# Performance work log

Hardware: AMD Instinct MI355X
Metric: run time of the kernel (lower is better)

Reference implementation:

```python
import jax, jax.numpy as jnp
import numpy as np

NV, NF, DIM = 6144, 12288, 256


def _linear(x, W, b):
    # torch nn.Linear: x @ W.T + b, W has shape (out, in)
    return x @ W.T + b


def _agg(X, A, Wf, bf, Wg, bg):
    # AGG: out_fc = Linear(A @ X); out_gagg = Linear(A @ out_fc)  (eval mode: dropout is identity)
    out_fc = _linear(A @ X, Wf, bf)
    out_g = _linear(A @ out_fc, Wg, bg)
    return jax.nn.relu(out_fc + out_g)


def setup_inputs() -> dict:
    key = jax.random.key(0)
    ks = jax.random.split(key, 18)
    primal = jax.random.normal(ks[0], (NV, DIM), jnp.float32)
    # degree-normalized adjacency (docstring): scale uniform entries by 1/N for stable row sums
    A_primal = jax.random.uniform(ks[1], (NV, NV), jnp.float32) * (1.0 / NV)
    A_dual = jax.random.uniform(ks[2], (NF, NF), jnp.float32) * (1.0 / NF)
    A = jax.random.uniform(ks[3], (NV, NF), jnp.float32) * (1.0 / NF)
    faces = jax.random.randint(ks[4], (NF, 3), 0, NV)

    w = lambda k, shp: jax.random.normal(k, shp, jnp.float32) * 0.05
    return {
        "primal": primal, "A_primal": A_primal, "A_dual": A_dual, "A": A, "faces": faces,
        # 3 primal AGG layers (fc + gagg), stacked on leading axis
        "pW": w(ks[5], (3, DIM, DIM)), "pb": w(ks[6], (3, DIM)),
        "pgW": w(ks[7], (3, DIM, DIM)), "pgb": w(ks[8], (3, DIM)),
        # 3 dual AGG layers
        "dW": w(ks[9], (3, DIM, DIM)), "db": w(ks[10], (3, DIM)),
        "dgW": w(ks[11], (3, DIM, DIM)), "dgb": w(ks[12], (3, DIM)),
        # PDF linears: (dim, 2*dim)
        "Wp": w(ks[13], (DIM, 2 * DIM)), "bp": w(ks[14], (DIM,)),
        "Wd": w(ks[15], (DIM, 2 * DIM)), "bd": w(ks[16], (DIM,)),
    }


def reference(primal, A_primal, A_dual, A, faces, pW, pb, pgW, pgb, dW, db, dgW, dgb, Wp, bp, Wd, bd):
    x_p = primal
    x_d = (1.0 / 3.0) * (A.T @ primal)  # primal_dual
    primal_outs, dual_outs = [], []
    for i in range(3):
        primal_outs.append(x_p)
        x_p = _agg(x_p, A_primal, pW[i], pb[i], pgW[i], pgb[i]) + x_p
    for i in range(3):
        dual_outs.append(x_d)
        x_d = _agg(x_d, A_dual, dW[i], db[i], dgW[i], dgb[i]) + x_d
    # PDF: DAP gather-reduce  (N_f, 3, dim) -> (N_f, dim)
    f = jnp.mean(jnp.abs(x_p[faces] - x_d[:, None, :]), axis=1)
    out_dual = jax.nn.relu(_linear(jnp.concatenate([x_d, f], axis=1), Wd, bd))
    mapped = A @ f  # dual_primal
    out_primal = jax.nn.relu(_linear(jnp.concatenate([x_p, mapped], axis=1), Wp, bp))
    return (out_primal + x_p, out_dual + x_d, *primal_outs, *dual_outs)
```

## Files before the change

### kernel.cpp

```cpp
#include <hip/hip_runtime.h>


typedef short short8 __attribute__((ext_vector_type(8)));
typedef float floatx4 __attribute__((ext_vector_type(4)));
typedef unsigned short ushort4v __attribute__((ext_vector_type(4)));
typedef unsigned short u16;

#define DIMN 256
#define GBK 64

static const int kNV = 6144;
static const int kNF = 12288;
static const int SLAB = 768;

__device__ __forceinline__ float bf2f(u16 u) {
  union { unsigned int i; float f; } x; x.i = ((unsigned int)u) << 16; return x.f;
}
__device__ __forceinline__ u16 f2bf(float f) {
  union { float f; unsigned int i; } x; x.f = f;
  unsigned int r = x.i + 0x7fffu + ((x.i >> 16) & 1u);
  return (u16)(r >> 16);
}
__device__ __forceinline__ void gld_lds16(const void* g, void* l) {
  __builtin_amdgcn_global_load_lds((__attribute__((address_space(1))) void*)(g),
                                   (__attribute__((address_space(3))) void*)(l),
                                   16, 0, 0);
}

struct GJ {
  const void* A0; int A0mode; int lda0;
  const void* A1; int A1mode; int lda1; int K1;
  const void* Bt; int Btis32; int ldb;
  u16* P; int M; int nx; int kchunk;
  int fused;
  const float* bias; const u16* addmat; int do_relu;
  const float* resid; float* outf; u16* out16; u16* outT;
};
struct FJ {
  const u16* P; int S; int Mrows; float scale; float* out; u16* out16;
};

__device__ __forceinline__ void gemm_dev(const GJ& j, int bid)
{
  __shared__ __align__(16) u16 As[2][128 * GBK];
  __shared__ __align__(16) u16 Bs[2][128 * GBK];

  const int y = bid & 1;
  const int bx = (bid >> 1) % j.nx;
  const int bz = (bid >> 1) / j.nx;
  const int m0 = bx << 7;
  const int n0 = y << 7;
  const int kb = bz * j.kchunk;
  const int nkt = j.kchunk / GBK;

  const int tid = threadIdx.x;
  const int wid = tid >> 6;
  const int lane = tid & 63;
  const int wr = wid >> 1, wc = wid & 1;
  const int srow = lane >> 3;
  const int skk = (lane & 7) << 3;

  floatx4 acc[4][4];
  floatx4 zz = {0.f, 0.f, 0.f, 0.f};
#pragma unroll
  for (int i = 0; i < 4; ++i)
#pragma unroll
    for (int jj = 0; jj < 4; ++jj) acc[i][jj] = zz;

  auto stage = [&](int buf, int k0) {
    const void* base; int lda, mode, kl;
    if (k0 < j.K1) { base = j.A0; lda = j.lda0; mode = j.A0mode; kl = k0; }
    else           { base = j.A1; lda = j.lda1; mode = j.A1mode; kl = k0 - j.K1; }
    if (mode == 0) {
      const u16* U = (const u16*)base;
#pragma unroll
      for (int q = 0; q < 4; ++q) {
        int c = (wid << 2) + q;
        gld_lds16(U + (size_t)(m0 + (c << 3) + srow) * lda + kl + skk,
                  (void*)&As[buf][c << 9]);
      }
    } else {
      const float* F = (const float*)base;
#pragma unroll
      for (int q = 0; q < 4; ++q) {
        int c = (wid << 2) + q;
        const size_t gi = (size_t)(m0 + (c << 3) + srow) * lda + kl + skk;
        floatx4 f0 = *(const floatx4*)(F + gi);
        floatx4 f1 = *(const floatx4*)(F + gi + 4);
        short8 v;
#pragma unroll
        for (int e = 0; e < 4; ++e) { v[e] = (short)f2bf(f0[e]); v[4 + e] = (short)f2bf(f1[e]); }
        *(short8*)&As[buf][(c << 9) + (lane << 3)] = v;
      }
    }
    if (j.Btis32) {
      const float* F = (const float*)j.Bt;
#pragma unroll
      for (int q = 0; q < 4; ++q) {
        int c = (wid << 2) + q;
        const size_t gi = (size_t)(n0 + (c << 3) + srow) * j.ldb + k0 + skk;
        floatx4 f0 = *(const floatx4*)(F + gi);
        floatx4 f1 = *(const floatx4*)(F + gi + 4);
        short8 v;
#pragma unroll
        for (int e = 0; e < 4; ++e) { v[e] = (short)f2bf(f0[e]); v[4 + e] = (short)f2bf(f1[e]); }
        *(short8*)&Bs[buf][(c << 9) + (lane << 3)] = v;
      }
    } else {
      const u16* U = (const u16*)j.Bt;
#pragma unroll
      for (int q = 0; q < 4; ++q) {
        int c = (wid << 2) + q;
        gld_lds16(U + (size_t)(n0 + (c << 3) + srow) * j.ldb + k0 + skk,
                  (void*)&Bs[buf][c << 9]);
      }
    }
  };

  int cur = 0;
  stage(0, kb);
  for (int kt = 0; kt < nkt; ++kt) {
    __syncthreads();
    if (kt + 1 < nkt) stage(cur ^ 1, kb + (kt + 1) * GBK);
#pragma unroll
    for (int ks = 0; ks < 2; ++ks) {
      short8 a[4], b[4];
      const int ko = (ks << 5) + ((lane >> 4) << 3);
#pragma unroll
      for (int mi = 0; mi < 4; ++mi)
        a[mi] = *(const short8*)&As[cur][((wr << 6) + (mi << 4) + (lane & 15)) * GBK + ko];
#pragma unroll
      for (int ni = 0; ni < 4; ++ni)
        b[ni] = *(const short8*)&Bs[cur][((wc << 6) + (ni << 4) + (lane & 15)) * GBK + ko];
#pragma unroll
      for (int mi = 0; mi < 4; ++mi)
#pragma unroll
        for (int ni = 0; ni < 4; ++ni)
          acc[mi][ni] = __builtin_amdgcn_mfma_f32_16x16x32_bf16(a[mi], b[ni], acc[mi][ni], 0, 0, 0);
    }
    cur ^= 1;
  }

  if (j.fused) {
    u16* ts = (u16*)&As[0][0];
    if (j.outT) __syncthreads();
#pragma unroll
    for (int mi = 0; mi < 4; ++mi) {
#pragma unroll
      for (int ni = 0; ni < 4; ++ni) {
        const int ml0 = (wr << 6) + (mi << 4) + ((lane >> 4) << 2);
        const int nl = (wc << 6) + (ni << 4) + (lane & 15);
        const int n = n0 + nl;
        const float bv = j.bias ? j.bias[n] : 0.f;
#pragma unroll
        for (int r = 0; r < 4; ++r) {
          const int ml = ml0 + r;
          const size_t idx = (size_t)(m0 + ml) * DIMN + n;
          float t = acc[mi][ni][r] + bv;
          if (j.addmat) t += bf2f(j.addmat[idx]);
          if (j.do_relu) t = fmaxf(t, 0.f);
          if (j.resid) t += j.resid[idx];
          if (j.outf) j.outf[idx] = t;
          const u16 q = f2bf(t);
          if (j.out16) j.out16[idx] = q;
          if (j.outT) ts[ml * 128 + (nl ^ ((ml & 7) << 3))] = q;
        }
      }
    }
    if (j.outT) {
      __syncthreads();
      const int nl = tid >> 1;
      const int mh = (tid & 1) << 6;
#pragma unroll
      for (int c8 = 0; c8 < 8; ++c8) {
        const int mB = mh + (c8 << 3);
        short8 v;
#pragma unroll
        for (int e = 0; e < 8; ++e)
          v[e] = (short)ts[(mB + e) * 128 + (nl ^ (((mB + e) & 7) << 3))];
        *(short8*)&j.outT[(size_t)(n0 + nl) * j.M + (m0 + mB)] = v;
      }
    }
  } else {
    u16* Pz = j.P + (size_t)bz * (size_t)j.M * DIMN;
#pragma unroll
    for (int mi = 0; mi < 4; ++mi) {
#pragma unroll
      for (int ni = 0; ni < 4; ++ni) {
        const int mb = m0 + (wr << 6) + (mi << 4) + ((lane >> 4) << 2);
        const int n = n0 + (wc << 6) + (ni << 4) + (lane & 15);
#pragma unroll
        for (int r = 0; r < 4; ++r)
          Pz[(size_t)(mb + r) * DIMN + n] = f2bf(acc[mi][ni][r]);
      }
    }
  }
}

__global__ __launch_bounds__(256, 2) void gemm1_k(GJ j0) { gemm_dev(j0, blockIdx.x); }
__global__ __launch_bounds__(256, 2) void gemm2_k(GJ j0, GJ j1, int nb0) {
  if ((int)blockIdx.x < nb0) gemm_dev(j0, blockIdx.x);
  else                       gemm_dev(j1, blockIdx.x - nb0);
}

__device__ __forceinline__ void fin_dev(const FJ& f, int bid)
{
  const size_t MN = (size_t)f.Mrows * DIMN;
  const size_t i4 = (((size_t)bid << 8) + threadIdx.x) * 4;
  if (i4 >= MN) return;
  floatx4 v = {0.f, 0.f, 0.f, 0.f};
  for (int s = 0; s < f.S; ++s) {
    ushort4v p4 = *(const ushort4v*)(f.P + (size_t)s * MN + i4);
#pragma unroll
    for (int q = 0; q < 4; ++q) v[q] += bf2f(p4[q]);
  }
  floatx4 o;
#pragma unroll
  for (int q = 0; q < 4; ++q) o[q] = v[q] * f.scale;
  if (f.out) *(floatx4*)(f.out + i4) = o;
  if (f.out16) {
    unsigned long long qq = 0;
#pragma unroll
    for (int q = 0; q < 4; ++q) qq |= ((unsigned long long)f2bf(o[q])) << (16 * q);
    *(unsigned long long*)(f.out16 + i4) = qq;
  }
}
__global__ __launch_bounds__(256) void fin1_k(FJ f0) { fin_dev(f0, blockIdx.x); }
__global__ __launch_bounds__(256) void fin2_k(FJ f0, FJ f1, int nb0) {
  if ((int)blockIdx.x < nb0) fin_dev(f0, blockIdx.x);
  else                       fin_dev(f1, blockIdx.x - nb0);
}

__global__ __launch_bounds__(256)
void finalize_tr_k(const u16* __restrict__ P, int S, int Mrows, float scale,
                   float* __restrict__ outf, u16* __restrict__ outT, int ldT)
{
  __shared__ __align__(16) u16 t[64][64];
  const size_t MN = (size_t)Mrows * DIMN;
  const int r0 = blockIdx.x << 6;
  const int c0 = blockIdx.y << 6;
  const int tid = threadIdx.x;
  const int lr = tid >> 3;
  const int lc = (tid & 7) << 3;
#pragma unroll
  for (int h = 0; h < 2; ++h) {
    const int r = lr + (h << 5);
    const size_t gi = (size_t)(r0 + r) * DIMN + (c0 + lc);
    float a[8];
#pragma unroll
    for (int e = 0; e < 8; ++e) a[e] = 0.f;
    for (int s = 0; s < S; ++s) {
      short8 p = *(const short8*)(P + (size_t)s * MN + gi);
#pragma unroll
      for (int e = 0; e < 8; ++e) a[e] += bf2f((u16)p[e]);
    }
    short8 v;
    floatx4 o0, o1;
#pragma unroll
    for (int e = 0; e < 4; ++e) {
      o0[e] = a[e] * scale; o1[e] = a[4 + e] * scale;
      v[e] = (short)f2bf(o0[e]); v[4 + e] = (short)f2bf(o1[e]);
    }
    *(floatx4*)(outf + gi) = o0;
    *(floatx4*)(outf + gi + 4) = o1;
    *(short8*)&t[r][lc ^ ((r >> 3) << 3)] = v;
  }
  __syncthreads();
#pragma unroll
  for (int h = 0; h < 2; ++h) {
    const int oc = lr + (h << 5);
    short8 v;
#pragma unroll
    for (int e = 0; e < 8; ++e)
      v[e] = (short)t[lc + e][oc ^ ((lc >> 3) << 3)];
    *(short8*)&outT[(size_t)(c0 + oc) * ldT + (r0 + lc)] = v;
  }
}

__device__ __forceinline__ void transpose_dev(const void* in, int is32, int ldin,
                                              u16* out, int ldout, u16* copy16,
                                              int bx, int by)
{
  __shared__ __align__(16) u16 t[64][64];
  const int c0 = bx << 6;
  const int r0 = by << 6;
  const int tid = threadIdx.x;
  const int lr = tid >> 3;
  const int lc = (tid & 7) << 3;
#pragma unroll
  for (int h = 0; h < 2; ++h) {
    const int r = lr + (h << 5);
    short8 v;
    if (is32) {
      const float* F = (const float*)in;
      const size_t gi = (size_t)(r0 + r) * ldin + (c0 + lc);
      floatx4 f0 = *(const floatx4*)(F + gi);
      floatx4 f1 = *(const floatx4*)(F + gi + 4);
#pragma unroll
      for (int e = 0; e < 4; ++e) { v[e] = (short)f2bf(f0[e]); v[4 + e] = (short)f2bf(f1[e]); }
      if (copy16) *(short8*)(copy16 + gi) = v;
    } else {
      v = *(const short8*)((const u16*)in + (size_t)(r0 + r) * ldin + (c0 + lc));
    }
    *(short8*)&t[r][lc ^ ((r >> 3) << 3)] = v;
  }
  __syncthreads();
#pragma unroll
  for (int h = 0; h < 2; ++h) {
    const int oc = lr + (h << 5);
    short8 v;
#pragma unroll
    for (int e = 0; e < 8; ++e)
      v[e] = (short)t[lc + e][oc ^ ((lc >> 3) << 3)];
    *(short8*)&out[(size_t)(c0 + oc) * ldout + (r0 + lc)] = v;
  }
}

__global__ __launch_bounds__(256)
void transpose_k(const void* __restrict__ in, int is32, int ldin,
                 u16* __restrict__ out, int ldout, u16* __restrict__ copy16)
{
  transpose_dev(in, is32, ldin, out, ldout, copy16, blockIdx.x, blockIdx.y);
}

__device__ __forceinline__ void cvt_dev(const float* in, u16* out, size_t n,
                                        int bid, int nb)
{
  const size_t stride = (size_t)nb * 2048;
  for (size_t i = (((size_t)bid << 8) + threadIdx.x) << 3; i < n; i += stride) {
    floatx4 f0 = *(const floatx4*)(in + i);
    floatx4 f1 = *(const floatx4*)(in + i + 4);
    short8 v;
#pragma unroll
    for (int e = 0; e < 4; ++e) { v[e] = (short)f2bf(f0[e]); v[4 + e] = (short)f2bf(f1[e]); }
    *(short8*)(out + i) = v;
  }
}
__global__ __launch_bounds__(256)
void prep_k(const float* __restrict__ Ad, u16* __restrict__ Ad16,
            const float* __restrict__ Ap, u16* __restrict__ Ap16,
            const float* __restrict__ A, u16* __restrict__ At16, u16* __restrict__ A16,
            const float* __restrict__ primal, u16* __restrict__ XTp,
            float* __restrict__ pouts)
{
  const int bid = blockIdx.x;
  if (bid < 2048) {
    cvt_dev(Ad, Ad16, (size_t)kNF * kNF, bid, 2048);
  } else if (bid < 3072) {
    cvt_dev(Ap, Ap16, (size_t)kNV * kNV, bid - 2048, 1024);
  } else if (bid < 21504) {
    const int t = bid - 3072;
    transpose_dev(A, 1, kNF, At16, kNV, A16, t % 192, t / 192);
  } else if (bid < 21888) {
    const int t = bid - 21504;
    transpose_dev(primal, 1, DIMN, XTp, kNV, nullptr, t % 4, t / 4);
  } else {
    const int t = bid - 21888;
    const size_t i = (((size_t)t << 8) + threadIdx.x) << 3;
    *(floatx4*)(pouts + i) = *(const floatx4*)(primal + i);
    *(floatx4*)(pouts + i + 4) = *(const floatx4*)(primal + i + 4);
  }
}

__global__ __launch_bounds__(256)
void face_gather_tr_k(const float* __restrict__ xp, const float* __restrict__ xd,
                      const int* __restrict__ faces, u16* __restrict__ f,
                      u16* __restrict__ fT)
{
  __shared__ u16 tile[64][DIMN + 8];
  const int fi0 = blockIdx.x << 6;
  const int jj = threadIdx.x;
  for (int k = 0; k < 64; ++k) {
    const int fi = fi0 + k;
    const int a = faces[fi * 3 + 0];
    const int b = faces[fi * 3 + 1];
    const int c = faces[fi * 3 + 2];
    const float xv = xd[(size_t)fi * DIMN + jj];
    const float s = fabsf(xp[(size_t)a * DIMN + jj] - xv)
                  + fabsf(xp[(size_t)b * DIMN + jj] - xv)
                  + fabsf(xp[(size_t)c * DIMN + jj] - xv);
    const u16 q = f2bf(s * (1.0f / 3.0f));
    f[(size_t)fi * DIMN + jj] = q;
    tile[k][jj] = q;
  }
  __syncthreads();
#pragma unroll
  for (int c8 = 0; c8 < 8; ++c8) {
    short8 v;
#pragma unroll
    for (int e = 0; e < 8; ++e) v[e] = (short)tile[(c8 << 3) + e][jj];
    *(short8*)&fT[(size_t)jj * kNF + fi0 + (c8 << 3)] = v;
  }
}

extern "C" void kernel_launch(void* const* d_in, const int* in_sizes, int n_in,
                              void* d_out, int out_size, void* d_ws, size_t ws_size,
                              hipStream_t stream)
{
  (void)in_sizes; (void)n_in; (void)out_size;
  const float* primal   = (const float*)d_in[0];
  const float* A_primal = (const float*)d_in[1];
  const float* A_dual   = (const float*)d_in[2];
  const float* A        = (const float*)d_in[3];
  const int* faces      = (const int*)d_in[4];
  const float* pW  = (const float*)d_in[5];
  const float* pb  = (const float*)d_in[6];
  const float* pgW = (const float*)d_in[7];
  const float* pgb = (const float*)d_in[8];
  const float* dW  = (const float*)d_in[9];
  const float* db  = (const float*)d_in[10];
  const float* dgW = (const float*)d_in[11];
  const float* dgb = (const float*)d_in[12];
  const float* Wp  = (const float*)d_in[13];
  const float* bp  = (const float*)d_in[14];
  const float* Wd  = (const float*)d_in[15];
  const float* bd  = (const float*)d_in[16];

  char* wsp = (char*)d_ws;
  auto alloc = [&](size_t bytes) -> void* {
    void* p = (void*)wsp;
    wsp += (bytes + 255) & ~(size_t)255;
    return p;
  };
  const size_t NVD = (size_t)kNV * DIMN, NFD = (size_t)kNF * DIMN;
  u16* XTp   = (u16*)alloc(NVD * 2);
  u16* XTd   = (u16*)alloc(NFD * 2);
  u16* TBd   = (u16*)alloc(NFD * 2);
  u16* TBp   = (u16*)alloc(NVD * 2);
  u16* t1d   = (u16*)alloc(NFD * 2);
  u16* t1p   = (u16*)alloc(NVD * 2);
  u16* fcd   = (u16*)alloc(NFD * 2);
  u16* fcp   = (u16*)alloc(NVD * 2);
  float* xp3 = (float*)alloc(NVD * 4);
  float* xd3 = (float*)alloc(NFD * 4);
  u16* P     = (u16*)alloc((size_t)8 * NFD * 2);
  u16* Pd    = P;
  u16* Pp    = P + 4 * NFD;
  const size_t bigElems = (size_t)kNF * kNF + 2 * (size_t)kNF * kNV + (size_t)kNV * kNV;
  const size_t need = (size_t)(wsp - (char*)d_ws) + bigElems * 2 + 4096;
  const bool big = ws_size >= need;
  u16 *Ad16 = nullptr, *At16 = nullptr, *A16 = nullptr, *Ap16 = nullptr;
  if (big) {
    Ad16 = (u16*)alloc((size_t)kNF * kNF * 2);
    At16 = (u16*)alloc((size_t)kNF * kNV * 2);
    A16  = (u16*)alloc((size_t)kNV * kNF * 2);
    Ap16 = (u16*)alloc((size_t)kNV * kNV * 2);
  }

  float* out0  = (float*)d_out;
  float* out1  = out0 + NVD;
  float* pouts = out1 + NFD;
  float* douts = pouts + 3 * NVD;

  auto GP = [&](const void* A0, int mode, int lda, const u16* Bt, int ldb,
                u16* Pr, int M, int K, int S) -> GJ {
    GJ g{}; g.A0 = A0; g.A0mode = mode; g.lda0 = lda;
    g.A1 = nullptr; g.A1mode = 0; g.lda1 = 0; g.K1 = K;
    g.Bt = Bt; g.Btis32 = 0; g.ldb = ldb;
    g.P = Pr; g.M = M; g.nx = M / 128; g.kchunk = K / S; g.fused = 0;
    g.bias = nullptr; g.addmat = nullptr; g.do_relu = 0; g.resid = nullptr;
    g.outf = nullptr; g.out16 = nullptr; g.outT = nullptr;
    return g;
  };
  auto GF = [&](const void* A0, int a0m, int lda0, const void* A1, int a1m,
                int lda1, int K1, const void* Bt, int bt32, int ldb, int M, int K,
                const float* bias, const u16* add, int relu, const float* resid,
                float* outf, u16* out16, u16* outT) -> GJ {
    GJ g{}; g.A0 = A0; g.A0mode = a0m; g.lda0 = lda0;
    g.A1 = A1; g.A1mode = a1m; g.lda1 = lda1; g.K1 = K1;
    g.Bt = Bt; g.Btis32 = bt32; g.ldb = ldb;
    g.P = P; g.M = M; g.nx = M / 128; g.kchunk = K; g.fused = 1;
    g.bias = bias; g.addmat = add; g.do_relu = relu; g.resid = resid;
    g.outf = outf; g.out16 = out16; g.outT = outT;
    return g;
  };
  auto gblk = [&](const GJ& g) { return g.nx * 2 * (g.fused ? 1 : (g.K1 / g.kchunk)); };
  auto launch2 = [&](const GJ& a, const GJ& b) {
    const int nb0 = gblk(a);
    gemm2_k<<<dim3(nb0 + gblk(b)), dim3(256), 0, stream>>>(a, b, nb0);
  };
  auto launch1 = [&](const GJ& a) {
    gemm1_k<<<dim3(gblk(a)), dim3(256), 0, stream>>>(a);
  };
  auto FIN = [&](const u16* Pr, int S, int M, float scale, float* out, u16* out16) -> FJ {
    FJ f{}; f.P = Pr; f.S = S; f.Mrows = M; f.scale = scale; f.out = out; f.out16 = out16;
    return f;
  };
  auto fblk = [&](const FJ& f) { return (int)((size_t)f.Mrows * DIMN / 1024); };
  auto fin2 = [&](const FJ& a, const FJ& b) {
    const int nb0 = fblk(a);
    fin2_k<<<dim3(nb0 + fblk(b)), dim3(256), 0, stream>>>(a, b, nb0);
  };
  auto fin1 = [&](const FJ& a) { fin1_k<<<dim3(fblk(a)), dim3(256), 0, stream>>>(a); };
  auto tranp = [&](const void* in, int is32, int ldin, u16* out, int ldout,
                   int R, int C, u16* copy16) {
    transpose_k<<<dim3(C / 64, R / 64), dim3(256), 0, stream>>>(
        in, is32, ldin, out, ldout, copy16);
  };

  if (big) {
    prep_k<<<dim3(22656), dim3(256), 0, stream>>>(
        A_dual, Ad16, A_primal, Ap16, A, At16, A16, primal, XTp, pouts);
  } else {
    tranp(primal, 1, DIMN, XTp, kNV, kNV, DIMN, nullptr);
    hipMemcpyAsync(pouts, primal, NVD * 4, hipMemcpyDeviceToDevice, stream);
  }

  const void* ApP = big ? (const void*)Ap16 : (const void*)A_primal;
  const int apm = big ? 0 : 1;
  const void* AdP = big ? (const void*)Ad16 : (const void*)A_dual;
  const int adm = big ? 0 : 1;

  if (big) {
    launch1(GP(At16, 0, kNV, XTp, kNV, Pd, kNF, kNV, 4));
    finalize_tr_k<<<dim3(kNF / 64, 4), dim3(256), 0, stream>>>(
        Pd, 4, kNF, 1.0f / 3.0f, douts, XTd, kNF);
  } else {
    for (int s = 0; s < kNF / SLAB; ++s) {
      const int m0 = s * SLAB;
      tranp(A + m0, 1, kNF, TBd, kNV, kNV, SLAB, nullptr);
      launch1(GP(TBd, 0, kNV, XTp, kNV, Pd, SLAB, kNV, 16));
      fin1(FIN(Pd, 16, SLAB, 1.0f / 3.0f, douts + (size_t)m0 * DIMN, nullptr));
    }
    tranp(douts, 1, DIMN, XTd, kNF, kNF, DIMN, nullptr);
  }

  const float* xpc = primal;
  const float* xdc = douts;
  for (int i = 0; i < 3; ++i) {
    launch2(GP(AdP, adm, kNF, XTd, kNF, Pd, kNF, kNF, 4),
            GP(ApP, apm, kNV, XTp, kNV, Pp, kNV, kNV, 8));
    fin2(FIN(Pd, 4, kNF, 1.f, nullptr, t1d), FIN(Pp, 8, kNV, 1.f, nullptr, t1p));
    launch2(GF(t1d, 0, 256, nullptr, 0, 0, 256, dW + (size_t)i * 65536, 1, 256,
               kNF, 256, db + i * 256, nullptr, 0, nullptr, nullptr, fcd, TBd),
            GF(t1p, 0, 256, nullptr, 0, 0, 256, pW + (size_t)i * 65536, 1, 256,
               kNV, 256, pb + i * 256, nullptr, 0, nullptr, nullptr, fcp, TBp));
    launch2(GP(AdP, adm, kNF, TBd, kNF, Pd, kNF, kNF, 4),
            GP(ApP, apm, kNV, TBp, kNV, Pp, kNV, kNV, 8));
    fin2(FIN(Pd, 4, kNF, 1.f, nullptr, t1d), FIN(Pp, 8, kNV, 1.f, nullptr, t1p));
    float* nxd = (i < 2) ? (douts + (size_t)(i + 1) * NFD) : xd3;
    float* nxp = (i < 2) ? (pouts + (size_t)(i + 1) * NVD) : xp3;
    u16* xdT = (i < 2) ? XTd : nullptr;
    u16* xpT = (i < 2) ? XTp : nullptr;
    launch2(GF(t1d, 0, 256, nullptr, 0, 0, 256, dgW + (size_t)i * 65536, 1, 256,
               kNF, 256, dgb + i * 256, fcd, 1, xdc, nxd, nullptr, xdT),
            GF(t1p, 0, 256, nullptr, 0, 0, 256, pgW + (size_t)i * 65536, 1, 256,
               kNV, 256, pgb + i * 256, fcp, 1, xpc, nxp, nullptr, xpT));
    xdc = nxd; xpc = nxp;
  }

  face_gather_tr_k<<<dim3(kNF / 64), dim3(256), 0, stream>>>(
      xp3, xd3, faces, t1d, TBd);
  {
    GJ jo = GF(xd3, 1, 256, t1d, 0, 256, 256, Wd, 1, 512, kNF, 512,
               bd, nullptr, 1, xd3, out1, nullptr, nullptr);
    GJ jm = big ? GP(A16, 0, kNF, TBd, kNF, Pp, kNV, kNF, 8)
                : GP(A, 1, kNF, TBd, kNF, Pp, kNV, kNF, 8);
    launch2(jo, jm);
  }
  fin1(FIN(Pp, 8, kNV, 1.f, nullptr, fcp));
  launch1(GF(xp3, 1, 256, fcp, 0, 256, 256, Wp, 1, 512, kNV, 512,
             bp, nullptr, 1, xp3, out0, nullptr, nullptr));
}
```

Measured before the change: 1.800 ms.

## Fuse the whole post-prep pipeline into one persistent cooperative kernel with grid syncs

Replaces the sequence of roughly twenty GEMM, finalize, face-gather and transpose launches with a single persistent cooperative kernel. That kernel loops over virtual blocks for each stage and separates stages with a threadfence and grid.sync. Shared memory becomes one 64KB buffer passed into the device functions, with __syncthreads added before reuse. The goal is to remove per-launch overhead and tail gaps between small kernels. In exchange the grid is capped at 256 or 512 blocks, which may leave load imbalance within stages, and the kernel falls back to the old path if the cooperative launch fails.

```diff
diff --git a/kernel.cpp b/kernel.cpp
--- a/kernel.cpp
+++ b/kernel.cpp
@@ -1,5 +1,8 @@
 #include <hip/hip_runtime.h>
-
+#include <hip/hip_cooperative_groups.h>
+
+
+namespace cg = cooperative_groups;
 
 typedef short short8 __attribute__((ext_vector_type(8)));
 typedef float floatx4 __attribute__((ext_vector_type(4)));
@@ -40,10 +43,41 @@
   const u16* P; int S; int Mrows; float scale; float* out; u16* out16;
 };
 
-__device__ __forceinline__ void gemm_dev(const GJ& j, int bid)
-{
-  __shared__ __align__(16) u16 As[2][128 * GBK];
-  __shared__ __align__(16) u16 Bs[2][128 * GBK];
+__device__ __forceinline__ GJ mkGP(const void* A0, int mode, int lda, const u16* Bt,
+                                   int ldb, u16* Pr, int M, int K, int S) {
+  GJ g; g.A0 = A0; g.A0mode = mode; g.lda0 = lda;
+  g.A1 = nullptr; g.A1mode = 0; g.lda1 = 0; g.K1 = K;
+  g.Bt = Bt; g.Btis32 = 0; g.ldb = ldb;
+  g.P = Pr; g.M = M; g.nx = M / 128; g.kchunk = K / S; g.fused = 0;
+  g.bias = nullptr; g.addmat = nullptr; g.do_relu = 0; g.resid = nullptr;
+  g.outf = nullptr; g.out16 = nullptr; g.outT = nullptr;
+  return g;
+}
+__device__ __forceinline__ GJ mkGF(const void* A0, int a0m, int lda0, const void* A1,
+                                   int a1m, int lda1, int K1, const void* Bt, int bt32,
+                                   int ldb, int M, int K, const float* bias,
+                                   const u16* add, int relu, const float* resid,
+                                   float* outf, u16* out16, u16* outT) {
+  GJ g; g.A0 = A0; g.A0mode = a0m; g.lda0 = lda0;
+  g.A1 = A1; g.A1mode = a1m; g.lda1 = lda1; g.K1 = K1;
+  g.Bt = Bt; g.Btis32 = bt32; g.ldb = ldb;
+  g.P = nullptr; g.M = M; g.nx = M / 128; g.kchunk = K; g.fused = 1;
+  g.bias = bias; g.addmat = add; g.do_relu = relu; g.resid = resid;
+  g.outf = outf; g.out16 = out16; g.outT = outT;
+  return g;
+}
+__device__ __forceinline__ FJ mkFIN(const u16* Pr, int S, int M, float scale,
+                                    float* out, u16* out16) {
+  FJ f; f.P = Pr; f.S = S; f.Mrows = M; f.scale = scale; f.out = out; f.out16 = out16;
+  return f;
+}
+
+__device__ __forceinline__ void gemm_dev(const GJ& j, int bid, char* smbase)
+{
+  u16* As = (u16*)smbase;
+  u16* Bs = (u16*)(smbase + 32768);
+
+  __syncthreads();
 
   const int y = bid & 1;
   const int bx = (bid >> 1) % j.nx;
@@ -77,7 +111,7 @@
       for (int q = 0; q < 4; ++q) {
         int c = (wid << 2) + q;
         gld_lds16(U + (size_t)(m0 + (c << 3) + srow) * lda + kl + skk,
-                  (void*)&As[buf][c << 9]);
+                  (void*)&As[buf * 8192 + (c << 9)]);
       }
     } else {
       const float* F = (const float*)base;
@@ -90,7 +124,7 @@
         short8 v;
 #pragma unroll
         for (int e = 0; e < 4; ++e) { v[e] = (short)f2bf(f0[e]); v[4 + e] = (short)f2bf(f1[e]); }
-        *(short8*)&As[buf][(c << 9) + (lane << 3)] = v;
+        *(short8*)&As[buf * 8192 + (c << 9) + (lane << 3)] = v;
       }
     }
     if (j.Btis32) {
@@ -104,7 +138,7 @@
         short8 v;
 #pragma unroll
         for (int e = 0; e < 4; ++e) { v[e] = (short)f2bf(f0[e]); v[4 + e] = (short)f2bf(f1[e]); }
-        *(short8*)&Bs[buf][(c << 9) + (lane << 3)] = v;
+        *(short8*)&Bs[buf * 8192 + (c << 9) + (lane << 3)] = v;
       }
     } else {
       const u16* U = (const u16*)j.Bt;
@@ -112,7 +146,7 @@
       for (int q = 0; q < 4; ++q) {
         int c = (wid << 2) + q;
         gld_lds16(U + (size_t)(n0 + (c << 3) + srow) * j.ldb + k0 + skk,
-                  (void*)&Bs[buf][c << 9]);
+                  (void*)&Bs[buf * 8192 + (c << 9)]);
       }
     }
   };
@@ -128,10 +162,10 @@
       const int ko = (ks << 5) + ((lane >> 4) << 3);
 #pragma unroll
       for (int mi = 0; mi < 4; ++mi)
-        a[mi] = *(const short8*)&As[cur][((wr << 6) + (mi << 4) + (lane & 15)) * GBK + ko];
+        a[mi] = *(const short8*)&As[cur * 8192 + ((wr << 6) + (mi << 4) + (lane & 15)) * GBK + ko];
 #pragma unroll
       for (int ni = 0; ni < 4; ++ni)
-        b[ni] = *(const short8*)&Bs[cur][((wc << 6) + (ni << 4) + (lane & 15)) * GBK + ko];
+        b[ni] = *(const short8*)&Bs[cur * 8192 + ((wc << 6) + (ni << 4) + (lane & 15)) * GBK + ko];
 #pragma unroll
       for (int mi = 0; mi < 4; ++mi)
 #pragma unroll
@@ -142,7 +176,7 @@
   }
 
   if (j.fused) {
-    u16* ts = (u16*)&As[0][0];
+    u16* ts = (u16*)smbase;
     if (j.outT) __syncthreads();
 #pragma unroll
     for (int mi = 0; mi < 4; ++mi) {
@@ -197,10 +231,14 @@
   }
 }
 
-__global__ __launch_bounds__(256, 2) void gemm1_k(GJ j0) { gemm_dev(j0, blockIdx.x); }
+__global__ __launch_bounds__(256, 2) void gemm1_k(GJ j0) {
+  __shared__ __align__(16) char sm[65536];
+  gemm_dev(j0, blockIdx.x, sm);
+}
 __global__ __launch_bounds__(256, 2) void gemm2_k(GJ j0, GJ j1, int nb0) {
-  if ((int)blockIdx.x < nb0) gemm_dev(j0, blockIdx.x);
-  else                       gemm_dev(j1, blockIdx.x - nb0);
+  __shared__ __align__(16) char sm[65536];
+  if ((int)blockIdx.x < nb0) gemm_dev(j0, blockIdx.x, sm);
+  else                       gemm_dev(j1, blockIdx.x - nb0, sm);
 }
 
 __device__ __forceinline__ void fin_dev(const FJ& f, int bid)
@@ -231,14 +269,15 @@
   else                       fin_dev(f1, blockIdx.x - nb0);
 }
 
-__global__ __launch_bounds__(256)
-void finalize_tr_k(const u16* __restrict__ P, int S, int Mrows, float scale,
-                   float* __restrict__ outf, u16* __restrict__ outT, int ldT)
-{
-  __shared__ __align__(16) u16 t[64][64];
+__device__ __forceinline__ void fin_tr_dev(const u16* P, int S, int Mrows, float scale,
+                                           float* outf, u16* outT, int ldT,
+                                           char* smbase, int bx, int by)
+{
+  u16 (*t)[64] = (u16 (*)[64])smbase;
+  __syncthreads();
   const size_t MN = (size_t)Mrows * DIMN;
-  const int r0 = blockIdx.x << 6;
-  const int c0 = blockIdx.y << 6;
+  const int r0 = bx << 6;
+  const int c0 = by << 6;
   const int tid = threadIdx.x;
   const int lr = tid >> 3;
   const int lc = (tid & 7) << 3;
@@ -276,12 +315,19 @@
     *(short8*)&outT[(size_t)(c0 + oc) * ldT + (r0 + lc)] = v;
   }
 }
+__global__ __launch_bounds__(256)
+void finalize_tr_k(const u16* __restrict__ P, int S, int Mrows, float scale,
+                   float* __restrict__ outf, u16* __restrict__ outT, int ldT)
+{
+  __shared__ __align__(16) char sm[8192];
+  fin_tr_dev(P, S, Mrows, scale, outf, outT, ldT, sm, blockIdx.x, blockIdx.y);
+}
 
 __device__ __forceinline__ void transpose_dev(const void* in, int is32, int ldin,
                                               u16* out, int ldout, u16* copy16,
-                                              int bx, int by)
-{
-  __shared__ __align__(16) u16 t[64][64];
+                                              int bx, int by, char* smbase)
+{
+  u16 (*t)[64] = (u16 (*)[64])smbase;
   const int c0 = bx << 6;
   const int r0 = by << 6;
   const int tid = threadIdx.x;
@@ -315,12 +361,12 @@
     *(short8*)&out[(size_t)(c0 + oc) * ldout + (r0 + lc)] = v;
   }
 }
-
 __global__ __launch_bounds__(256)
 void transpose_k(const void* __restrict__ in, int is32, int ldin,
                  u16* __restrict__ out, int ldout, u16* __restrict__ copy16)
 {
-  transpose_dev(in, is32, ldin, out, ldout, copy16, blockIdx.x, blockIdx.y);
+  __shared__ __align__(16) char sm[8192];
+  transpose_dev(in, is32, ldin, out, ldout, copy16, blockIdx.x, blockIdx.y, sm);
 }
 
 __device__ __forceinline__ void cvt_dev(const float* in, u16* out, size_t n,
@@ -343,6 +389,7 @@
             const float* __restrict__ primal, u16* __restrict__ XTp,
             float* __restrict__ pouts)
 {
+  __shared__ __align__(16) char sm[8192];
   const int bid = blockIdx.x;
   if (bid < 2048) {
     cvt_dev(Ad, Ad16, (size_t)kNF * kNF, bid, 2048);
@@ -350,10 +397,10 @@
     cvt_dev(Ap, Ap16, (size_t)kNV * kNV, bid - 2048, 1024);
   } else if (bid < 21504) {
     const int t = bid - 3072;
-    transpose_dev(A, 1, kNF, At16, kNV, A16, t % 192, t / 192);
+    transpose_dev(A, 1, kNF, At16, kNV, A16, t % 192, t / 192, sm);
   } else if (bid < 21888) {
     const int t = bid - 21504;
-    transpose_dev(primal, 1, DIMN, XTp, kNV, nullptr, t % 4, t / 4);
+    transpose_dev(primal, 1, DIMN, XTp, kNV, nullptr, t % 4, t / 4, sm);
   } else {
     const int t = bid - 21888;
     const size_t i = (((size_t)t << 8) + threadIdx.x) << 3;
@@ -362,13 +409,13 @@
   }
 }
 
-__global__ __launch_bounds__(256)
-void face_gather_tr_k(const float* __restrict__ xp, const float* __restrict__ xd,
-                      const int* __restrict__ faces, u16* __restrict__ f,
-                      u16* __restrict__ fT)
-{
-  __shared__ u16 tile[64][DIMN + 8];
-  const int fi0 = blockIdx.x << 6;
+__device__ __forceinline__ void face_dev(const float* xp, const float* xd,
+                                         const int* faces, u16* f, u16* fT,
+                                         char* smbase, int bid)
+{
+  u16 (*tile)[DIMN + 8] = (u16 (*)[DIMN + 8])smbase;
+  __syncthreads();
+  const int fi0 = bid << 6;
   const int jj = threadIdx.x;
   for (int k = 0; k < 64; ++k) {
     const int fi = fi0 + k;
@@ -391,6 +438,117 @@
     for (int e = 0; e < 8; ++e) v[e] = (short)tile[(c8 << 3) + e][jj];
     *(short8*)&fT[(size_t)jj * kNF + fi0 + (c8 << 3)] = v;
   }
+}
+__global__ __launch_bounds__(256)
+void face_gather_tr_k(const float* __restrict__ xp, const float* __restrict__ xd,
+                      const int* __restrict__ faces, u16* __restrict__ f,
+                      u16* __restrict__ fT)
+{
+  __shared__ __align__(16) char sm[33792];
+  face_dev(xp, xd, faces, f, fT, sm, blockIdx.x);
+}
+
+struct MegaArgs {
+  const u16 *Ad16, *Ap16, *At16, *A16;
+  u16 *XTp, *XTd, *TBd, *TBp, *t1d, *t1p, *fcd, *fcp;
+  float *xp3, *xd3;
+  u16 *Pd, *Pp;
+  const float *pW, *pb, *pgW, *pgb, *dW, *db, *dgW, *dgb, *Wp, *bp, *Wd, *bd;
+  const int* faces;
+  const float* primal;
+  float *pouts, *douts, *out0, *out1;
+};
+
+__global__ __launch_bounds__(256, 2) void mega_k(MegaArgs a)
+{
+  __shared__ __align__(16) char sm[65536];
+  cg::grid_group grid = cg::this_grid();
+  const int nb = (int)gridDim.x;
+  const size_t NVD = (size_t)kNV * DIMN, NFD = (size_t)kNF * DIMN;
+
+  auto gsync = [&]() { __threadfence(); grid.sync(); };
+
+  for (int vb = blockIdx.x; vb < 768; vb += nb)
+    gemm_dev(mkGP(a.At16, 0, kNV, a.XTp, kNV, a.Pd, kNF, kNV, 4), vb, sm);
+  gsync();
+  for (int vb = blockIdx.x; vb < 768; vb += nb)
+    fin_tr_dev(a.Pd, 4, kNF, 1.0f / 3.0f, a.douts, a.XTd, kNF, sm, vb % 192, vb / 192);
+  gsync();
+
+  const float* xdc = a.douts;
+  const float* xpc = a.primal;
+  for (int i = 0; i < 3; ++i) {
+    const float* dWi = a.dW + (size_t)i * 65536;
+    const float* dgWi = a.dgW + (size_t)i * 65536;
+    const float* pWi = a.pW + (size_t)i * 65536;
+    const float* pgWi = a.pgW + (size_t)i * 65536;
+    const float* dbi = a.db + i * 256;
+    const float* dgbi = a.dgb + i * 256;
+    const float* pbi = a.pb + i * 256;
+    const float* pgbi = a.pgb + i * 256;
+
+    for (int vb = blockIdx.x; vb < 1536; vb += nb) {
+      if (vb < 768) gemm_dev(mkGP(a.Ad16, 0, kNF, a.XTd, kNF, a.Pd, kNF, kNF, 4), vb, sm);
+      else          gemm_dev(mkGP(a.Ap16, 0, kNV, a.XTp, kNV, a.Pp, kNV, kNV, 8), vb - 768, sm);
+    }
+    gsync();
+    for (int vb = blockIdx.x; vb < 4608; vb += nb) {
+      if (vb < 3072) fin_dev(mkFIN(a.Pd, 4, kNF, 1.f, nullptr, a.t1d), vb);
+      else           fin_dev(mkFIN(a.Pp, 8, kNV, 1.f, nullptr, a.t1p), vb - 3072);
+    }
+    gsync();
+    for (int vb = blockIdx.x; vb < 288; vb += nb) {
+      if (vb < 192)
+        gemm_dev(mkGF(a.t1d, 0, 256, nullptr, 0, 0, 256, dWi, 1, 256, kNF, 256,
+                      dbi, nullptr, 0, nullptr, nullptr, a.fcd, a.TBd), vb, sm);
+      else
+        gemm_dev(mkGF(a.t1p, 0, 256, nullptr, 0, 0, 256, pWi, 1, 256, kNV, 256,
+                      pbi, nullptr, 0, nullptr, nullptr, a.fcp, a.TBp), vb - 192, sm);
+    }
+    gsync();
+    for (int vb = blockIdx.x; vb < 1536; vb += nb) {
+      if (vb < 768) gemm_dev(mkGP(a.Ad16, 0, kNF, a.TBd, kNF, a.Pd, kNF, kNF, 4), vb, sm);
+      else          gemm_dev(mkGP(a.Ap16, 0, kNV, a.TBp, kNV, a.Pp, kNV, kNV, 8), vb - 768, sm);
+    }
+    gsync();
+    for (int vb = blockIdx.x; vb < 4608; vb += nb) {
+      if (vb < 3072) fin_dev(mkFIN(a.Pd, 4, kNF, 1.f, nullptr, a.t1d), vb);
+      else           fin_dev(mkFIN(a.Pp, 8, kNV, 1.f, nullptr, a.t1p), vb - 3072);
+    }
+    gsync();
+    float* nxd = (i < 2) ? (a.douts + (size_t)(i + 1) * NFD) : a.xd3;
+    float* nxp = (i < 2) ? (a.pouts + (size_t)(i + 1) * NVD) : a.xp3;
+    u16* xdT = (i < 2) ? a.XTd : nullptr;
+    u16* xpT = (i < 2) ? a.XTp : nullptr;
+    for (int vb = blockIdx.x; vb < 288; vb += nb) {
+      if (vb < 192)
+        gemm_dev(mkGF(a.t1d, 0, 256, nullptr, 0, 0, 256, dgWi, 1, 256, kNF, 256,
+                      dgbi, a.fcd, 1, xdc, nxd, nullptr, xdT), vb, sm);
+      else
+        gemm_dev(mkGF(a.t1p, 0, 256, nullptr, 0, 0, 256, pgWi, 1, 256, kNV, 256,
+                      pgbi, a.fcp, 1, xpc, nxp, nullptr, xpT), vb - 192, sm);
+    }
+    gsync();
+    xdc = nxd; xpc = nxp;
+  }
+
+  for (int vb = blockIdx.x; vb < 192; vb += nb)
+    face_dev(a.xp3, a.xd3, a.faces, a.t1d, a.TBd, sm, vb);
+  gsync();
+  for (int vb = blockIdx.x; vb < 960; vb += nb) {
+    if (vb < 192)
+      gemm_dev(mkGF(a.xd3, 1, 256, a.t1d, 0, 256, 256, a.Wd, 1, 512, kNF, 512,
+                    a.bd, nullptr, 1, a.xd3, a.out1, nullptr, nullptr), vb, sm);
+    else
+      gemm_dev(mkGP(a.A16, 0, kNF, a.TBd, kNF, a.Pp, kNV, kNF, 8), vb - 192, sm);
+  }
+  gsync();
+  for (int vb = blockIdx.x; vb < 1536; vb += nb)
+    fin_dev(mkFIN(a.Pp, 8, kNV, 1.f, nullptr, a.fcp), vb);
+  gsync();
+  for (int vb = blockIdx.x; vb < 96; vb += nb)
+    gemm_dev(mkGF(a.xp3, 1, 256, a.fcp, 0, 256, 256, a.Wp, 1, 512, kNV, 512,
+                  a.bp, nullptr, 1, a.xp3, a.out0, nullptr, nullptr), vb, sm);
 }
 
 extern "C" void kernel_launch(void* const* d_in, const int* in_sizes, int n_in,
@@ -452,113 +610,140 @@
   float* pouts = out1 + NFD;
   float* douts = pouts + 3 * NVD;
 
-  auto GP = [&](const void* A0, int mode, int lda, const u16* Bt, int ldb,
-                u16* Pr, int M, int K, int S) -> GJ {
-    GJ g{}; g.A0 = A0; g.A0mode = mode; g.lda0 = lda;
-    g.A1 = nullptr; g.A1mode = 0; g.lda1 = 0; g.K1 = K;
-    g.Bt = Bt; g.Btis32 = 0; g.ldb = ldb;
-    g.P = Pr; g.M = M; g.nx = M / 128; g.kchunk = K / S; g.fused = 0;
-    g.bias = nullptr; g.addmat = nullptr; g.do_relu = 0; g.resid = nullptr;
-    g.outf = nullptr; g.out16 = nullptr; g.outT = nullptr;
-    return g;
-  };
-  auto GF = [&](const void* A0, int a0m, int lda0, const void* A1, int a1m,
-                int lda1, int K1, const void* Bt, int bt32, int ldb, int M, int K,
-                const float* bias, const u16* add, int relu, const float* resid,
-                float* outf, u16* out16, u16* outT) -> GJ {
-    GJ g{}; g.A0 = A0; g.A0mode = a0m; g.lda0 = lda0;
-    g.A1 = A1; g.A1mode = a1m; g.lda1 = lda1; g.K1 = K1;
-    g.Bt = Bt; g.Btis32 = bt32; g.ldb = ldb;
-    g.P = P; g.M = M; g.nx = M / 128; g.kchunk = K; g.fused = 1;
-    g.bias = bias; g.addmat = add; g.do_relu = relu; g.resid = resid;
-    g.outf = outf; g.out16 = out16; g.outT = outT;
-    return g;
-  };
-  auto gblk = [&](const GJ& g) { return g.nx * 2 * (g.fused ? 1 : (g.K1 / g.kchunk)); };
-  auto launch2 = [&](const GJ& a, const GJ& b) {
-    const int nb0 = gblk(a);
-    gemm2_k<<<dim3(nb0 + gblk(b)), dim3(256), 0, stream>>>(a, b, nb0);
-  };
-  auto launch1 = [&](const GJ& a) {
-    gemm1_k<<<dim3(gblk(a)), dim3(256), 0, stream>>>(a);
-  };
-  auto FIN = [&](const u16* Pr, int S, int M, float scale, float* out, u16* out16) -> FJ {
-    FJ f{}; f.P = Pr; f.S = S; f.Mrows = M; f.scale = scale; f.out = out; f.out16 = out16;
-    return f;
-  };
-  auto fblk = [&](const FJ& f) { return (int)((size_t)f.Mrows * DIMN / 1024); };
-  auto fin2 = [&](const FJ& a, const FJ& b) {
-    const int nb0 = fblk(a);
-    fin2_k<<<dim3(nb0 + fblk(b)), dim3(256), 0, stream>>>(a, b, nb0);
-  };
-  auto fin1 = [&](const FJ& a) { fin1_k<<<dim3(fblk(a)), dim3(256), 0, stream>>>(a); };
-  auto tranp = [&](const void* in, int is32, int ldin, u16* out, int ldout,
-                   int R, int C, u16* copy16) {
-    transpose_k<<<dim3(C / 64, R / 64), dim3(256), 0, stream>>>(
-        in, is32, ldin, out, ldout, copy16);
-  };
-
   if (big) {
     prep_k<<<dim3(22656), dim3(256), 0, stream>>>(
         A_dual, Ad16, A_primal, Ap16, A, At16, A16, primal, XTp, pouts);
-  } else {
-    tranp(primal, 1, DIMN, XTp, kNV, kNV, DIMN, nullptr);
-    hipMemcpyAsync(pouts, primal, NVD * 4, hipMemcpyDeviceToDevice, stream);
-  }
-
-  const void* ApP = big ? (const void*)Ap16 : (const void*)A_primal;
-  const int apm = big ? 0 : 1;
-  const void* AdP = big ? (const void*)Ad16 : (const void*)A_dual;
-  const int adm = big ? 0 : 1;
-
+  }
+
+  bool useMega = false;
   if (big) {
-    launch1(GP(At16, 0, kNV, XTp, kNV, Pd, kNF, kNV, 4));
-    finalize_tr_k<<<dim3(kNF / 64, 4), dim3(256), 0, stream>>>(
-        Pd, 4, kNF, 1.0f / 3.0f, douts, XTd, kNF);
-  } else {
-    for (int s = 0; s < kNF / SLAB; ++s) {
-      const int m0 = s * SLAB;
-      tranp(A + m0, 1, kNF, TBd, kNV, kNV, SLAB, nullptr);
-      launch1(GP(TBd, 0, kNV, XTp, kNV, Pd, SLAB, kNV, 16));
-      fin1(FIN(Pd, 16, SLAB, 1.0f / 3.0f, douts + (size_t)m0 * DIMN, nullptr));
-    }
-    tranp(douts, 1, DIMN, XTd, kNF, kNF, DIMN, nullptr);
-  }
-
-  const float* xpc = primal;
-  const float* xdc = douts;
-  for (int i = 0; i < 3; ++i) {
-    launch2(GP(AdP, adm, kNF, XTd, kNF, Pd, kNF, kNF, 4),
-            GP(ApP, apm, kNV, XTp, kNV, Pp, kNV, kNV, 8));
-    fin2(FIN(Pd, 4, kNF, 1.f, nullptr, t1d), FIN(Pp, 8, kNV, 1.f, nullptr, t1p));
-    launch2(GF(t1d, 0, 256, nullptr, 0, 0, 256, dW + (size_t)i * 65536, 1, 256,
-               kNF, 256, db + i * 256, nullptr, 0, nullptr, nullptr, fcd, TBd),
-            GF(t1p, 0, 256, nullptr, 0, 0, 256, pW + (size_t)i * 65536, 1, 256,
-               kNV, 256, pb + i * 256, nullptr, 0, nullptr, nullptr, fcp, TBp));
-    launch2(GP(AdP, adm, kNF, TBd, kNF, Pd, kNF, kNF, 4),
-            GP(ApP, apm, kNV, TBp, kNV, Pp, kNV, kNV, 8));
-    fin2(FIN(Pd, 4, kNF, 1.f, nullptr, t1d), FIN(Pp, 8, kNV, 1.f, nullptr, t1p));
-    float* nxd = (i < 2) ? (douts + (size_t)(i + 1) * NFD) : xd3;
-    float* nxp = (i < 2) ? (pouts + (size_t)(i + 1) * NVD) : xp3;
-    u16* xdT = (i < 2) ? XTd : nullptr;
-    u16* xpT = (i < 2) ? XTp : nullptr;
-    launch2(GF(t1d, 0, 256, nullptr, 0, 0, 256, dgW + (size_t)i * 65536, 1, 256,
-               kNF, 256, dgb + i * 256, fcd, 1, xdc, nxd, nullptr, xdT),
-            GF(t1p, 0, 256, nullptr, 0, 0, 256, pgW + (size_t)i * 65536, 1, 256,
-               kNV, 256, pgb + i * 256, fcp, 1, xpc, nxp, nullptr, xpT));
-    xdc = nxd; xpc = nxp;
-  }
-
-  face_gather_tr_k<<<dim3(kNF / 64), dim3(256), 0, stream>>>(
-      xp3, xd3, faces, t1d, TBd);
-  {
-    GJ jo = GF(xd3, 1, 256, t1d, 0, 256, 256, Wd, 1, 512, kNF, 512,
-               bd, nullptr, 1, xd3, out1, nullptr, nullptr);
-    GJ jm = big ? GP(A16, 0, kNF, TBd, kNF, Pp, kNV, kNF, 8)
-                : GP(A, 1, kNF, TBd, kNF, Pp, kNV, kNF, 8);
-    launch2(jo, jm);
-  }
-  fin1(FIN(Pp, 8, kNV, 1.f, nullptr, fcp));
-  launch1(GF(xp3, 1, 256, fcp, 0, 256, 256, Wp, 1, 512, kNV, 512,
-             bp, nullptr, 1, xp3, out0, nullptr, nullptr));
-}
+    MegaArgs ma;
+    ma.Ad16 = Ad16; ma.Ap16 = Ap16; ma.At16 = At16; ma.A16 = A16;
+    ma.XTp = XTp; ma.XTd = XTd; ma.TBd = TBd; ma.TBp = TBp;
+    ma.t1d = t1d; ma.t1p = t1p; ma.fcd = fcd; ma.fcp = fcp;
+    ma.xp3 = xp3; ma.xd3 = xd3; ma.Pd = Pd; ma.Pp = Pp;
+    ma.pW = pW; ma.pb = pb; ma.pgW = pgW; ma.pgb = pgb;
+    ma.dW = dW; ma.db = db; ma.dgW = dgW; ma.dgb = dgb;
+    ma.Wp = Wp; ma.bp = bp; ma.Wd = Wd; ma.bd = bd;
+    ma.faces = faces; ma.primal = primal;
+    ma.pouts = pouts; ma.douts = douts; ma.out0 = out0; ma.out1 = out1;
+    int maxb = 0;
+    if (hipOccupancyMaxActiveBlocksPerMultiprocessor(&maxb, mega_k, 256, 0)
+            == hipSuccess && maxb >= 1) {
+      const int nblk = (maxb >= 2 ? 512 : 256);
+      void* kp[1] = { &ma };
+      if (hipLaunchCooperativeKernel((void*)mega_k, dim3(nblk), dim3(256),
+                                     kp, 0, stream) == hipSuccess)
+        useMega = true;
+    }
+  }
+
+  if (!useMega) {
+    auto GP = [&](const void* A0, int mode, int lda, const u16* Bt, int ldb,
+                  u16* Pr, int M, int K, int S) -> GJ {
+      GJ g{}; g.A0 = A0; g.A0mode = mode; g.lda0 = lda;
+      g.A1 = nullptr; g.A1mode = 0; g.lda1 = 0; g.K1 = K;
+      g.Bt = Bt; g.Btis32 = 0; g.ldb = ldb;
+      g.P = Pr; g.M = M; g.nx = M / 128; g.kchunk = K / S; g.fused = 0;
+      g.bias = nullptr; g.addmat = nullptr; g.do_relu = 0; g.resid = nullptr;
+      g.outf = nullptr; g.out16 = nullptr; g.outT = nullptr;
+      return g;
+    };
+    auto GF = [&](const void* A0, int a0m, int lda0, const void* A1, int a1m,
+                  int lda1, int K1, const void* Bt, int bt32, int ldb, int M, int K,
+                  const float* bias, const u16* add, int relu, const float* resid,
+                  float* outf, u16* out16, u16* outT) -> GJ {
+      GJ g{}; g.A0 = A0; g.A0mode = a0m; g.lda0 = lda0;
+      g.A1 = A1; g.A1mode = a1m; g.lda1 = lda1; g.K1 = K1;
+      g.Bt = Bt; g.Btis32 = bt32; g.ldb = ldb;
+      g.P = P; g.M = M; g.nx = M / 128; g.kchunk = K; g.fused = 1;
+      g.bias = bias; g.addmat = add; g.do_relu = relu; g.resid = resid;
+      g.outf = outf; g.out16 = out16; g.outT = outT;
+      return g;
+    };
+    auto gblk = [&](const GJ& g) { return g.nx * 2 * (g.fused ? 1 : (g.K1 / g.kchunk)); };
+    auto launch2 = [&](const GJ& aj, const GJ& bj) {
+      const int nb0 = gblk(aj);
+      gemm2_k<<<dim3(nb0 + gblk(bj)), dim3(256), 0, stream>>>(aj, bj, nb0);
+    };
+    auto launch1 = [&](const GJ& aj) {
+      gemm1_k<<<dim3(gblk(aj)), dim3(256), 0, stream>>>(aj);
+    };
+    auto FIN = [&](const u16* Pr, int S, int M, float scale, float* out, u16* out16) -> FJ {
+      FJ f{}; f.P = Pr; f.S = S; f.Mrows = M; f.scale = scale; f.out = out; f.out16 = out16;
+      return f;
+    };
+    auto fblk = [&](const FJ& f) { return (int)((size_t)f.Mrows * DIMN / 1024); };
+    auto fin2 = [&](const FJ& aj, const FJ& bj) {
+      const int nb0 = fblk(aj);
+      fin2_k<<<dim3(nb0 + fblk(bj)), dim3(256), 0, stream>>>(aj, bj, nb0);
+    };
+    auto fin1 = [&](const FJ& aj) { fin1_k<<<dim3(fblk(aj)), dim3(256), 0, stream>>>(aj); };
+    auto tranp = [&](const void* in, int is32, int ldin, u16* out, int ldout,
+                     int R, int C, u16* copy16) {
+      transpose_k<<<dim3(C / 64, R / 64), dim3(256), 0, stream>>>(
+          in, is32, ldin, out, ldout, copy16);
+    };
+
+    if (!big) {
+      tranp(primal, 1, DIMN, XTp, kNV, kNV, DIMN, nullptr);
+      hipMemcpyAsync(pouts, primal, NVD * 4, hipMemcpyDeviceToDevice, stream);
+    }
+
+    const void* ApP = big ? (const void*)Ap16 : (const void*)A_primal;
+    const int apm = big ? 0 : 1;
+    const void* AdP = big ? (const void*)Ad16 : (const void*)A_dual;
+    const int adm = big ? 0 : 1;
+
+    if (big) {
+      launch1(GP(At16, 0, kNV, XTp, kNV, Pd, kNF, kNV, 4));
+      finalize_tr_k<<<dim3(kNF / 64, 4), dim3(256), 0, stream>>>(
+          Pd, 4, kNF, 1.0f / 3.0f, douts, XTd, kNF);
+    } else {
+      for (int s = 0; s < kNF / SLAB; ++s) {
+        const int m0 = s * SLAB;
+        tranp(A + m0, 1, kNF, TBd, kNV, kNV, SLAB, nullptr);
+        launch1(GP(TBd, 0, kNV, XTp, kNV, Pd, SLAB, kNV, 16));
+        fin1(FIN(Pd, 16, SLAB, 1.0f / 3.0f, douts + (size_t)m0 * DIMN, nullptr));
+      }
+      tranp(douts, 1, DIMN, XTd, kNF, kNF, DIMN, nullptr);
+    }
+
+    const float* xpc = primal;
+    const float* xdc = douts;
+    for (int i = 0; i < 3; ++i) {
+      launch2(GP(AdP, adm, kNF, XTd, kNF, Pd, kNF, kNF, 4),
+              GP(ApP, apm, kNV, XTp, kNV, Pp, kNV, kNV, 8));
+      fin2(FIN(Pd, 4, kNF, 1.f, nullptr, t1d), FIN(Pp, 8, kNV, 1.f, nullptr, t1p));
+      launch2(GF(t1d, 0, 256, nullptr, 0, 0, 256, dW + (size_t)i * 65536, 1, 256,
+                 kNF, 256, db + i * 256, nullptr, 0, nullptr, nullptr, fcd, TBd),
+              GF(t1p, 0, 256, nullptr, 0, 0, 256, pW + (size_t)i * 65536, 1, 256,
+                 kNV, 256, pb + i * 256, nullptr, 0, nullptr, nullptr, fcp, TBp));
+      launch2(GP(AdP, adm, kNF, TBd, kNF, Pd, kNF, kNF, 4),
+              GP(ApP, apm, kNV, TBp, kNV, Pp, kNV, kNV, 8));
+      fin2(FIN(Pd, 4, kNF, 1.f, nullptr, t1d), FIN(Pp, 8, kNV, 1.f, nullptr, t1p));
+      float* nxd = (i < 2) ? (douts + (size_t)(i + 1) * NFD) : xd3;
+      float* nxp = (i < 2) ? (pouts + (size_t)(i + 1) * NVD) : xp3;
+      u16* xdT = (i < 2) ? XTd : nullptr;
+      u16* xpT = (i < 2) ? XTp : nullptr;
+      launch2(GF(t1d, 0, 256, nullptr, 0, 0, 256, dgW + (size_t)i * 65536, 1, 256,
+                 kNF, 256, dgb + i * 256, fcd, 1, xdc, nxd, nullptr, xdT),
+              GF(t1p, 0, 256, nullptr, 0, 0, 256, pgW + (size_t)i * 65536, 1, 256,
+                 kNV, 256, pgb + i * 256, fcp, 1, xpc, nxp, nullptr, xpT));
+      xdc = nxd; xpc = nxp;
+    }
+
+    face_gather_tr_k<<<dim3(kNF / 64), dim3(256), 0, stream>>>(
+        xp3, xd3, faces, t1d, TBd);
+    {
+      GJ jo = GF(xd3, 1, 256, t1d, 0, 256, 256, Wd, 1, 512, kNF, 512,
+                 bd, nullptr, 1, xd3, out1, nullptr, nullptr);
+      GJ jm = big ? GP(A16, 0, kNF, TBd, kNF, Pp, kNV, kNF, 8)
+                  : GP(A, 1, kNF, TBd, kNF, Pp, kNV, kNF, 8);
+      launch2(jo, jm);
+    }
+    fin1(FIN(Pp, 8, kNV, 1.f, nullptr, fcp));
+    launch1(GF(xp3, 1, 256, fcp, 0, 256, 256, Wp, 1, 512, kNV, 512,
+               bp, nullptr, 1, xp3, out0, nullptr, nullptr));
+  }
+}
```

Result: slower. 3.611 ms (+100.6%).
